# Performance work log

Hardware: AMD Instinct MI355X
Metric: run time of the kernel (lower is better)

The kernel has to match this reference:

```python
import jax, jax.numpy as jnp
import numpy as np

N_CELLS_PER_SIDE = 16
MAX_K = 32
N_HEADS = 8
CHUNK = 128

_NEIGHBOR_OFFSETS = jnp.array([[-1, -1], [-1, 0], [-1, 1], [0, -1], [0, 0], [0, 1], [1, -1], [1, 0], [1, 1]], dtype=jnp.int32)


def cell_lookup(query_pos, cell_map, pos_min, pos_range):
    B, S, _ = query_pos.shape
    mpc = cell_map.shape[1]
    normalized = (query_pos - pos_min) / pos_range
    cell_xy = jnp.clip((normalized * N_CELLS_PER_SIDE).astype(jnp.int32), 0, N_CELLS_PER_SIDE - 1)
    nb = jnp.clip(cell_xy[:, :, None, :] + _NEIGHBOR_OFFSETS[None, None, :, :], 0, N_CELLS_PER_SIDE - 1)
    nidx = nb[..., 0] * N_CELLS_PER_SIDE + nb[..., 1]
    cand = cell_map[nidx].reshape(B, S, 9 * mpc)
    valid = cand >= 0
    return jnp.where(valid, cand, 0), valid


def threshold_gate(scores, tau, max_k):
    raw = scores - tau
    gate = jnp.where(raw > 0, raw, 1e-8 * jnp.exp(raw))
    eg = jnp.exp(gate) - 1.0
    k = min(max_k, scores.shape[-1])
    tv, _ = jax.lax.top_k(eg, k)
    eg = jnp.where(eg >= tv[:, :, -1:], eg, 0.0)
    gs = eg.sum(axis=-1, keepdims=True) + 1e-8
    strength = jnp.tanh(eg.max(axis=-1, keepdims=True))
    return eg / gs * strength


def setup_inputs() -> dict:
    key = jax.random.key(0)
    ks = jax.random.split(key, 16)
    B, S, D, N, P = 2, 1024, 512, 4096, 2
    n_cells, mpc = N_CELLS_PER_SIDE ** 2, 32
    return {
        "x": jax.random.normal(ks[0], (B, S, D), jnp.float32),
        "qk_pos": jax.random.uniform(ks[1], (B, S, P), jnp.float32),
        "v_pos": jax.random.uniform(ks[2], (B, S, P), jnp.float32),
        "tau_Q": jax.random.uniform(ks[3], (B, S, 1), jnp.float32),
        "tau_K": jax.random.uniform(ks[4], (B, S, 1), jnp.float32),
        "tau_V": jax.random.uniform(ks[5], (B, S, 1), jnp.float32),
        "qk_neurons": jax.random.normal(ks[6], (N, D), jnp.float32) / np.float32(np.sqrt(D)),
        "v_neurons": jax.random.normal(ks[7], (N, D), jnp.float32) / np.float32(np.sqrt(D)),
        "npos_qk": jax.random.uniform(ks[8], (N, P), jnp.float32),
        "npos_v": jax.random.uniform(ks[9], (N, P), jnp.float32),
        "cell_map_qk": jax.random.randint(ks[10], (n_cells, mpc), 0, N, jnp.int32),
        "cell_map_v": jax.random.randint(ks[11], (n_cells, mpc), 0, N, jnp.int32),
        "pos_min": jnp.zeros((P,), jnp.float32),
        "pos_range": jnp.ones((P,), jnp.float32),
        "expand_O": jax.random.normal(ks[12], (D, D), jnp.float32) * 0.02,
    }


def reference(x, qk_pos, v_pos, tau_Q, tau_K, tau_V, qk_neurons, v_neurons, npos_qk, npos_v, cell_map_qk, cell_map_v, pos_min, pos_range, expand_O):
    B, S, D = x.shape
    # full-sequence spatial cell lookup (small int tensors)
    ci_qk, m_qk = cell_lookup(qk_pos, cell_map_qk, pos_min, pos_range)
    ci_v, m_v = cell_lookup(v_pos, cell_map_v, pos_min, pos_range)
    ci_qk = jax.lax.stop_gradient(ci_qk)
    ci_v = jax.lax.stop_gradient(ci_v)
    nc = S // CHUNK  # S chosen divisible by CHUNK (no padding path needed)

    def chunks(a):
        return a.reshape(B, nc, CHUNK, *a.shape[2:]).swapaxes(0, 1)

    inp = tuple(map(chunks, (x, qk_pos, v_pos, tau_Q, tau_K, tau_V, ci_qk, m_qk, ci_v, m_v)))

    def step(carry, c):
        x_c, qkp, vp, tq, tk, tv, i_qk, mk, i_v, mv = c
        cand_qk = qk_neurons[i_qk]  # [B,C,n_cand,D]
        cand_v = v_neurons[i_v]
        act_qk = jnp.einsum('bsd,bsnd->bsn', x_c, cand_qk)
        act_v = jnp.einsum('bsd,bsnd->bsn', x_c, cand_v)
        s_qk = jnp.where(mk, act_qk, -1e9)
        s_v = jnp.where(mv, act_v, -1e9)
        gQ = threshold_gate(s_qk, tq, MAX_K)
        gK = threshold_gate(s_qk, tk, MAX_K)
        gV = threshold_gate(s_v, tv, MAX_K)
        Q_c = jnp.einsum('bsn,bsnd->bsd', act_qk * gQ * mk, cand_qk)
        K_c = jnp.einsum('bsn,bsnd->bsd', act_qk * gK * mk, cand_qk)
        V_c = jnp.einsum('bsn,bsnd->bsd', act_v * gV * mv, cand_v)
        pd_qk = jnp.sum((qkp[:, :, None, :] - npos_qk[i_qk]) ** 2, axis=-1)
        pl_qk = (jax.lax.stop_gradient(gQ) * pd_qk * mk).sum() / (mk.sum() + 1e-8)
        pd_v = jnp.sum((vp[:, :, None, :] - npos_v[i_v]) ** 2, axis=-1)
        pl_v = (jax.lax.stop_gradient(gV) * pd_v * mv).sum() / (mv.sum() + 1e-8)
        return carry, (Q_c, K_c, V_c, pl_qk + pl_v)

    _, (Qs, Ks, Vs, pls) = jax.lax.scan(step, 0, inp)

    def merge(a):
        return a.swapaxes(0, 1).reshape(B, S, D)

    Q, K, V = merge(Qs), merge(Ks), merge(Vs)
    pos_loss = pls.mean()  # == sum / n_chunks

    dh = D // N_HEADS
    Qh = Q.reshape(B, S, N_HEADS, dh).transpose(0, 2, 1, 3)
    Kh = K.reshape(B, S, N_HEADS, dh).transpose(0, 2, 1, 3)
    Vh = V.reshape(B, S, N_HEADS, dh).transpose(0, 2, 1, 3)
    scores = jnp.einsum('bhsd,bhtd->bhst', Qh, Kh) / jnp.sqrt(jnp.float32(dh))
    causal = jnp.tril(jnp.ones((S, S), dtype=jnp.bool_))
    scores = jnp.where(causal, scores, jnp.finfo(scores.dtype).min)
    attn = jax.nn.softmax(scores, axis=-1)
    out = jnp.einsum('bhst,bhtd->bhsd', attn, Vh)
    out = out.transpose(0, 2, 1, 3).reshape(B, S, D)
    out = out @ expand_O
    return out, pos_loss
```

## Files before the change

### kernel.cpp

```cpp
#include <hip/hip_runtime.h>
#include <math.h>

#define B_ 2
#define S_ 1024
#define D_ 512
#define N_ 4096
#define H_ 8
#define DH_ 64
#define NCAND 288
#define TOPK 32
#define NTOK (B_*S_)
#define NG2 1152

#define NROWS 16384
#define NSLOT_BH 8704
#define NSLOTS (16*NSLOT_BH)

__device__ __forceinline__ float wave_sum(float v) {
    #pragma unroll
    for (int o = 32; o; o >>= 1) v += __shfl_xor(v, o);
    return v;
}
__device__ __forceinline__ float wave_max(float v) {
    #pragma unroll
    for (int o = 32; o; o >>= 1) v = fmaxf(v, __shfl_xor(v, o));
    return v;
}

__global__ __launch_bounds__(1024) void sort_tokens_kernel(
    const float* __restrict__ qk_pos, const float* __restrict__ v_pos,
    const float* __restrict__ pos_min, const float* __restrict__ pos_range,
    int* __restrict__ order_qk, int* __restrict__ order_v,
    int2* __restrict__ desc_qk, int2* __restrict__ desc_v)
{
    __shared__ int hist[256], tmp[256], offs[256], startc[256], gcnt[256];
    const int t = threadIdx.x;
    const int pass = blockIdx.x;
    const float pm0 = pos_min[0], pm1 = pos_min[1];
    const float pr0 = pos_range[0], pr1 = pos_range[1];
    const float* pos = pass ? v_pos : qk_pos;
    int* order = pass ? order_v : order_qk;
    int2* desc = pass ? desc_v : desc_qk;
    if (t < NG2) desc[t] = make_int2(0, 0);
    if (t + 1024 < NG2) desc[t + 1024] = make_int2(0, 0);
    if (t < 256) hist[t] = 0;
    __syncthreads();
    int cell[2];
    #pragma unroll
    for (int k = 0; k < 2; k++) {
        int tok = t + k * 1024;
        float p0 = pos[tok * 2], p1 = pos[tok * 2 + 1];
        int cx = min(max((int)((p0 - pm0) / pr0 * 16.f), 0), 15);
        int cy = min(max((int)((p1 - pm1) / pr1 * 16.f), 0), 15);
        cell[k] = cx * 16 + cy;
        atomicAdd(&hist[cell[k]], 1);
    }
    __syncthreads();
    if (t < 256) tmp[t] = hist[t];
    __syncthreads();
    for (int d = 1; d < 256; d <<= 1) {
        int v = 0;
        if (t < 256 && t >= d) v = tmp[t - d];
        __syncthreads();
        if (t < 256) tmp[t] += v;
        __syncthreads();
    }
    if (t < 256) {
        startc[t] = tmp[t] - hist[t];
        offs[t]   = startc[t];
        gcnt[t]   = (hist[t] + 1) >> 1;
    }
    __syncthreads();
    #pragma unroll
    for (int k = 0; k < 2; k++) {
        int tok = t + k * 1024;
        int p = atomicAdd(&offs[cell[k]], 1);
        order[p] = tok;
    }
    __syncthreads();
    if (t < 256) tmp[t] = gcnt[t];
    __syncthreads();
    for (int d = 1; d < 256; d <<= 1) {
        int v = 0;
        if (t < 256 && t >= d) v = tmp[t - d];
        __syncthreads();
        if (t < 256) tmp[t] += v;
        __syncthreads();
    }
    if (t < 256) {
        int g0 = tmp[t] - gcnt[t];
        for (int k = 0; k < gcnt[t]; k++)
            desc[g0 + k] = make_int2(startc[t] + 2 * k, min(2, hist[t] - 2 * k));
    }
}

__global__ __launch_bounds__(256) void qkv_fused(
    const int2* __restrict__ desc_qk, const int* __restrict__ order_qk,
    const int2* __restrict__ desc_v,  const int* __restrict__ order_v,
    const float* __restrict__ x,
    const float* __restrict__ qk_pos, const float* __restrict__ v_pos,
    const float* __restrict__ tauQ, const float* __restrict__ tauK,
    const float* __restrict__ tauV,
    const float* __restrict__ qk_neurons, const float* __restrict__ v_neurons,
    const float* __restrict__ npos_qk, const float* __restrict__ npos_v,
    const int* __restrict__ cm_qk, const int* __restrict__ cm_v,
    const float* __restrict__ pos_min, const float* __restrict__ pos_range,
    float* __restrict__ Q, float* __restrict__ K, float* __restrict__ V,
    float* __restrict__ posacc)
{
    const int bid = blockIdx.x;
    const int role = bid & 1;
    const int g = bid >> 1;
    const int gid = (g & 7) * 144 + (g >> 3);
    const int2 dsc = role ? desc_v[gid] : desc_qk[gid];
    const int gstart = dsc.x, count = dsc.y;
    if (count == 0) return;

    const int*   order   = role ? order_v   : order_qk;
    const float* pose    = role ? v_pos     : qk_pos;
    const float* neurons = role ? v_neurons : qk_neurons;
    const float* npos    = role ? npos_v    : npos_qk;
    const int*   cmap    = role ? cm_v      : cm_qk;

    __shared__ int   idx[NCAND];
    __shared__ float msk[NCAND];
    __shared__ float act[2][NCAND];
    __shared__ int   ci[2][NCAND];
    __shared__ float cw1[2][NCAND], cw2[2][NCAND];
    __shared__ int   toks[2], cnt2[2];
    __shared__ float red[2][2][4];
    __shared__ float redc;

    const int t = threadIdx.x, wid = t >> 6, lane = t & 63;
    const int sub = lane & 15, grp = lane >> 4;
    if (t < 2) { toks[t] = order[gstart + min(t, count - 1)]; cnt2[t] = 0; }
    __syncthreads();
    const int token0 = toks[0];

    const float pm0 = pos_min[0], pm1 = pos_min[1];
    const float pr0 = pos_range[0], pr1 = pos_range[1];
    {
        const float p0 = pose[token0 * 2], p1 = pose[token0 * 2 + 1];
        const int cx = min(max((int)((p0 - pm0) / pr0 * 16.f), 0), 15);
        const int cy = min(max((int)((p1 - pm1) / pr1 * 16.f), 0), 15);
        for (int c = t; c < NCAND; c += 256) {
            int o = c >> 5, ms = c & 31;
            int nx = min(max(cx + o / 3 - 1, 0), 15), ny = min(max(cy + o % 3 - 1, 0), 15);
            int cand = cmap[(nx * 16 + ny) * 32 + ms];
            idx[c] = cand >= 0 ? cand : 0;
            msk[c] = cand >= 0 ? 1.f : 0.f;
        }
    }
    __syncthreads();

    float4 xr0[8], xr1[8];
    {
        const float4* xp0 = (const float4*)(x + (size_t)toks[0] * D_);
        const float4* xp1 = (const float4*)(x + (size_t)toks[1] * D_);
        #pragma unroll
        for (int k = 0; k < 8; k++) {
            xr0[k] = xp0[k * 16 + sub];
            xr1[k] = xp1[k * 16 + sub];
        }
    }

    const int cb = wid * 72;
    for (int u = 0; u < 72; u += 4) {
        const int c = cb + u + grp;
        const float4* rp = (const float4*)(neurons + (size_t)idx[c] * D_);
        float a0 = 0.f, a1 = 0.f, b0 = 0.f, b1 = 0.f;
        #pragma unroll
        for (int k = 0; k < 8; k += 2) {
            float4 r0 = rp[k * 16 + sub];
            float4 r1 = rp[(k + 1) * 16 + sub];
            a0 += xr0[k].x*r0.x + xr0[k].y*r0.y + xr0[k].z*r0.z + xr0[k].w*r0.w;
            a1 += xr1[k].x*r0.x + xr1[k].y*r0.y + xr1[k].z*r0.z + xr1[k].w*r0.w;
            b0 += xr0[k+1].x*r1.x + xr0[k+1].y*r1.y + xr0[k+1].z*r1.z + xr0[k+1].w*r1.w;
            b1 += xr1[k+1].x*r1.x + xr1[k+1].y*r1.y + xr1[k+1].z*r1.z + xr1[k+1].w*r1.w;
        }
        float f0 = a0 + b0, f1 = a1 + b1;
        #pragma unroll
        for (int o = 1; o <= 8; o <<= 1) {
            f0 += __shfl_xor(f0, o);
            f1 += __shfl_xor(f1, o);
        }
        if (sub == 0) {
            const float mv = msk[c];
            act[0][c] = (mv != 0.f) ? f0 : -1e9f;
            act[1][c] = (mv != 0.f) ? f1 : -1e9f;
        }
    }
    __syncthreads();

    const int tk = wid >> 1, sw = wid & 1, tt = t & 127;
    const int token = toks[tk];

    if (sw == 0) {
        unsigned ej[5];
        #pragma unroll
        for (int k = 0; k < 5; k++) {
            int j = lane + 64 * k;
            float f = (j < NCAND) ? act[tk][j] : -1e30f;
            unsigned uu = __float_as_uint(f);
            ej[k] = (uu & 0x80000000u) ? ~uu : (uu | 0x80000000u);
        }
        unsigned T = 0u;
        for (int bit = 31; bit >= 0; bit--) {
            const unsigned cand = T | (1u << bit);
            int c = 0;
            #pragma unroll
            for (int k = 0; k < 5; k++)
                c += __popcll(__ballot(ej[k] >= cand));
            if (c >= TOPK) T = cand;
        }
        int base = 0;
        const unsigned long long below = (lane == 0) ? 0ull
                                       : (~0ull >> (64 - lane));
        #pragma unroll
        for (int k = 0; k < 5; k++) {
            const unsigned long long mk2 = __ballot(ej[k] >= T);
            if (ej[k] >= T) {
                int pos = base + __popcll(mk2 & below);
                ci[tk][pos] = lane + 64 * k;
            }
            base += __popcll(mk2);
        }
        if (lane == 0) cnt2[tk] = base;
    }
    if (wid == 0) {
        float cmv = 0.f;
        for (int c = lane; c < NCAND; c += 64) cmv += msk[c];
        cmv = wave_sum(cmv);
        if (lane == 0) redc = cmv;
    }
    __syncthreads();
    const float cm = redc;
    const int n = cnt2[tk];

    if (role == 0) {
        const float tq = tauQ[token], tkk = tauK[token];
        float sQ = 0.f, sK = 0.f, mQ = 0.f, mK = 0.f;
        for (int p = tt; p < n; p += 128) {
            float s = act[tk][ci[tk][p]];
            float rq = s - tq;
            float gq = (rq > 0.f) ? rq : 1e-8f * __expf(rq);
            float egq = __expf(gq) - 1.f;
            float rk = s - tkk;
            float gk = (rk > 0.f) ? rk : 1e-8f * __expf(rk);
            float egk = __expf(gk) - 1.f;
            cw1[tk][p] = egq; cw2[tk][p] = egk;
            sQ += egq; sK += egk;
            mQ = fmaxf(mQ, egq); mK = fmaxf(mK, egk);
        }
        sQ = wave_sum(sQ); mQ = wave_max(mQ);
        sK = wave_sum(sK); mK = wave_max(mK);
        if (lane == 0) {
            red[tk][sw][0] = sQ; red[tk][sw][1] = mQ;
            red[tk][sw][2] = sK; red[tk][sw][3] = mK;
        }
        __syncthreads();
        const float scQ = tanhf(fmaxf(red[tk][0][1], red[tk][1][1]))
                        / (red[tk][0][0] + red[tk][1][0] + 1e-8f);
        const float scK = tanhf(fmaxf(red[tk][0][3], red[tk][1][3]))
                        / (red[tk][0][2] + red[tk][1][2] + 1e-8f);
        __syncthreads();

        const float qp0 = pose[token * 2], qp1 = pose[token * 2 + 1];
        float plq = 0.f;
        for (int p = tt; p < n; p += 128) {
            int e = ci[tk][p];
            int id = idx[e];
            float m = msk[e], a = act[tk][e];
            float gq = cw1[tk][p] * scQ;
            cw1[tk][p] = a * gq * m;
            cw2[tk][p] = a * cw2[tk][p] * scK * m;
            ci[tk][p] = id;
            float d0 = qp0 - npos[id * 2], d1 = qp1 - npos[id * 2 + 1];
            plq += gq * (d0 * d0 + d1 * d1) * m;
        }
        plq = wave_sum(plq);
        if (lane == 0) red[tk][sw][0] = plq;
        __syncthreads();
        if (tt == 0 && tk < count) {
            int chunk = (token & 1023) >> 7;
            atomicAdd(&posacc[chunk], red[tk][0][0] + red[tk][1][0]);
            atomicAdd(&posacc[8 + chunk], cm);
        }

        if (tk < count) {
            float4 qa = {0,0,0,0}, ka = {0,0,0,0};
            int p = 0;
            for (; p + 1 < n; p += 2) {
                const float4 rA = *(const float4*)(neurons + (size_t)ci[tk][p] * D_ + tt * 4);
                const float4 rB = *(const float4*)(neurons + (size_t)ci[tk][p + 1] * D_ + tt * 4);
                const float wA = cw1[tk][p], bA = cw2[tk][p];
                const float wB = cw1[tk][p + 1], bB = cw2[tk][p + 1];
                qa.x += wA * rA.x + wB * rB.x; qa.y += wA * rA.y + wB * rB.y;
                qa.z += wA * rA.z + wB * rB.z; qa.w += wA * rA.w + wB * rB.w;
                ka.x += bA * rA.x + bB * rB.x; ka.y += bA * rA.y + bB * rB.y;
                ka.z += bA * rA.z + bB * rB.z; ka.w += bA * rA.w + bB * rB.w;
            }
            if (p < n) {
                const float4 rA = *(const float4*)(neurons + (size_t)ci[tk][p] * D_ + tt * 4);
                const float wA = cw1[tk][p], bA = cw2[tk][p];
                qa.x += wA * rA.x; qa.y += wA * rA.y; qa.z += wA * rA.z; qa.w += wA * rA.w;
                ka.x += bA * rA.x; ka.y += bA * rA.y; ka.z += bA * rA.z; ka.w += bA * rA.w;
            }
            *(float4*)(Q + (size_t)token * D_ + tt * 4) = qa;
            *(float4*)(K + (size_t)token * D_ + tt * 4) = ka;
        }
    } else {
        const float tv = tauV[token];
        float sV = 0.f, mV = 0.f;
        for (int p = tt; p < n; p += 128) {
            float s = act[tk][ci[tk][p]];
            float rv = s - tv;
            float gv = (rv > 0.f) ? rv : 1e-8f * __expf(rv);
            float egv = __expf(gv) - 1.f;
            cw1[tk][p] = egv;
            sV += egv; mV = fmaxf(mV, egv);
        }
        sV = wave_sum(sV); mV = wave_max(mV);
        if (lane == 0) { red[tk][sw][0] = sV; red[tk][sw][1] = mV; }
        __syncthreads();
        const float scV = tanhf(fmaxf(red[tk][0][1], red[tk][1][1]))
                        / (red[tk][0][0] + red[tk][1][0] + 1e-8f);
        __syncthreads();

        const float vp0 = pose[token * 2], vp1 = pose[token * 2 + 1];
        float plv = 0.f;
        for (int p = tt; p < n; p += 128) {
            int e = ci[tk][p];
            int id = idx[e];
            float m = msk[e], a = act[tk][e];
            float gv = cw1[tk][p] * scV;
            cw1[tk][p] = a * gv * m;
            ci[tk][p] = id;
            float d0 = vp0 - npos[id * 2], d1 = vp1 - npos[id * 2 + 1];
            plv += gv * (d0 * d0 + d1 * d1) * m;
        }
        plv = wave_sum(plv);
        if (lane == 0) red[tk][sw][0] = plv;
        __syncthreads();
        if (tt == 0 && tk < count) {
            int chunk = (token & 1023) >> 7;
            atomicAdd(&posacc[16 + chunk], red[tk][0][0] + red[tk][1][0]);
            atomicAdd(&posacc[24 + chunk], cm);
        }

        if (tk < count) {
            float4 va = {0,0,0,0};
            int p = 0;
            for (; p + 1 < n; p += 2) {
                const float4 rA = *(const float4*)(neurons + (size_t)ci[tk][p] * D_ + tt * 4);
                const float4 rB = *(const float4*)(neurons + (size_t)ci[tk][p + 1] * D_ + tt * 4);
                const float wA = cw1[tk][p], wB = cw1[tk][p + 1];
                va.x += wA * rA.x + wB * rB.x; va.y += wA * rA.y + wB * rB.y;
                va.z += wA * rA.z + wB * rB.z; va.w += wA * rA.w + wB * rB.w;
            }
            if (p < n) {
                const float4 rA = *(const float4*)(neurons + (size_t)ci[tk][p] * D_ + tt * 4);
                const float wA = cw1[tk][p];
                va.x += wA * rA.x; va.y += wA * rA.y; va.z += wA * rA.z; va.w += wA * rA.w;
            }
            *(float4*)(V + (size_t)token * D_ + tt * 4) = va;
        }
    }
}

typedef __attribute__((ext_vector_type(8))) short short8;
typedef __attribute__((ext_vector_type(4))) float f32x4;

__device__ __forceinline__ ushort f2b_rn(float f) {
    unsigned u = __float_as_uint(f);
    return (ushort)((u + 0x7FFFu + ((u >> 16) & 1u)) >> 16);
}
__device__ __forceinline__ float b2f(ushort h) {
    return __uint_as_float(((unsigned)h) << 16);
}
__device__ __forceinline__ int swzi(int row, int c8) {
    return row * 64 + ((c8 ^ (row & 7)) << 3);
}

__global__ __launch_bounds__(256, 2) void attn_partial_kernel(
    const float* __restrict__ Q, const float* __restrict__ K,
    const float* __restrict__ V,
    float* __restrict__ pm, float* __restrict__ pl, float* __restrict__ po)
{
    const int xx = blockIdx.x & 7;
    int kq = blockIdx.x >> 3;
    const int bh = xx + 8 * (kq >= 72);
    kq = (kq >= 72) ? kq - 72 : kq;
    int rblk = 0;
    while (kq >= 2 * (rblk + 1)) { kq -= 2 * (rblk + 1); rblk++; }
    const int sp = kq;
    const int b = bh >> 3, h = bh & 7;
    const int j0 = sp * 64;
    const int rbase = rblk * 128;

    __shared__ __align__(16) ushort sKhi[64 * 64], sKlo[64 * 64];
    __shared__ __align__(16) ushort sVthi[64 * 64], sVtlo[64 * 64];
    __shared__ __align__(16) float sPool[8192];

    const int t = threadIdx.x;
    const int w = t >> 6, lane = t & 63;
    const int g = lane >> 4, ln = lane & 15;

    {
        const int srow = t >> 2, scol = (t & 3) << 4;
        const float* Kg = K + ((size_t)(b * S_ + j0 + srow)) * D_ + h * DH_ + scol;
        const float* Vg = V + ((size_t)(b * S_ + j0 + srow)) * D_ + h * DH_ + scol;
        union { float4 f4[4]; float f[16]; } kf, vf;
        kf.f4[0] = *(const float4*)(Kg);
        kf.f4[1] = *(const float4*)(Kg + 4);
        kf.f4[2] = *(const float4*)(Kg + 8);
        kf.f4[3] = *(const float4*)(Kg + 12);
        vf.f4[0] = *(const float4*)(Vg);
        vf.f4[1] = *(const float4*)(Vg + 4);
        vf.f4[2] = *(const float4*)(Vg + 8);
        vf.f4[3] = *(const float4*)(Vg + 12);
        union { uint4 d[2]; ushort u[16]; } uh, ul;
        #pragma unroll
        for (int i = 0; i < 16; i++) {
            uh.u[i] = f2b_rn(kf.f[i]);
            ul.u[i] = f2b_rn(kf.f[i] - b2f(uh.u[i]));
        }
        const int c8 = (t & 3) << 1;
        *(uint4*)&sKhi[swzi(srow, c8)]     = uh.d[0];
        *(uint4*)&sKhi[swzi(srow, c8 + 1)] = uh.d[1];
        *(uint4*)&sKlo[swzi(srow, c8)]     = ul.d[0];
        *(uint4*)&sKlo[swzi(srow, c8 + 1)] = ul.d[1];
        #pragma unroll
        for (int i = 0; i < 16; i++) sPool[srow * 65 + scol + i] = vf.f[i];
    }
    __syncthreads();
    {
        const int drow = t >> 2, kcol = (t & 3) << 4;
        union { uint4 d[2]; ushort u[16]; } uh, ul;
        #pragma unroll
        for (int i = 0; i < 16; i++) {
            const float f = sPool[(kcol + i) * 65 + drow];
            uh.u[i] = f2b_rn(f);
            ul.u[i] = f2b_rn(f - b2f(uh.u[i]));
        }
        const int c8 = (t & 3) << 1;
        *(uint4*)&sVthi[swzi(drow, c8)]     = uh.d[0];
        *(uint4*)&sVthi[swzi(drow, c8 + 1)] = uh.d[1];
        *(uint4*)&sVtlo[swzi(drow, c8)]     = ul.d[0];
        *(uint4*)&sVtlo[swzi(drow, c8 + 1)] = ul.d[1];
    }
    __syncthreads();

    const int wrow = rbase + w * 32;
    if (wrow + 31 < j0) return;

    ushort* sPw = (ushort*)sPool + w * 4096;

    short8 qhi[2][2], qlo[2][2];
    #pragma unroll
    for (int qt = 0; qt < 2; qt++) {
        const int qrow = wrow + qt * 16 + ln;
        const float* Qg = Q + ((size_t)(b * S_ + qrow)) * D_ + h * DH_ + g * 8;
        #pragma unroll
        for (int ds = 0; ds < 2; ds++) {
// ... 74 lines not shown
            const int c8 = kt * 2 + (g >> 1);
            const int idx = qrow * 64 + ((c8 ^ (qrow & 7)) << 3) + ((g & 1) << 2);
            *(uint2*)&sPw[idx] = h4.d;
            *(uint2*)&sPw[2048 + idx] = l4.d;
        }
        if (g == 0 && qg >= j0) {
            const int gr = qg >> 6;
            const size_t slot = (size_t)bh * NSLOT_BH + 32 * gr * (gr + 1)
                              + (size_t)(qg & 63) * (gr + 1) + sp;
            pm[slot] = mq; pl[slot] = lq;
        }
    }

    f32x4 ot[4][2];
    #pragma unroll
    for (int dt = 0; dt < 4; dt++)
        #pragma unroll
        for (int qt = 0; qt < 2; qt++)
            ot[dt][qt] = fzero;
    #pragma unroll
    for (int ks = 0; ks < 2; ks++) {
        short8 pfh[2], pfl[2];
        #pragma unroll
        for (int qt = 0; qt < 2; qt++) {
            const int qrow = qt * 16 + ln;
            const int idx = qrow * 64 + (((ks * 4 + g) ^ (qrow & 7)) << 3);
            pfh[qt] = *(const short8*)&sPw[idx];
            pfl[qt] = *(const short8*)&sPw[2048 + idx];
        }
        #pragma unroll
        for (int dt = 0; dt < 4; dt++) {
            const int drow = dt * 16 + ln;
            const short8 vh = *(const short8*)&sVthi[swzi(drow, ks * 4 + g)];
            const short8 vl = *(const short8*)&sVtlo[swzi(drow, ks * 4 + g)];
            #pragma unroll
            for (int qt = 0; qt < 2; qt++) {
                ot[dt][qt] = __builtin_amdgcn_mfma_f32_16x16x32_bf16(vh, pfh[qt], ot[dt][qt], 0, 0, 0);
                ot[dt][qt] = __builtin_amdgcn_mfma_f32_16x16x32_bf16(vh, pfl[qt], ot[dt][qt], 0, 0, 0);
                ot[dt][qt] = __builtin_amdgcn_mfma_f32_16x16x32_bf16(vl, pfh[qt], ot[dt][qt], 0, 0, 0);
            }
        }
    }

    #pragma unroll
    for (int qt = 0; qt < 2; qt++) {
        const int qg = wrow + qt * 16 + ln;
        if (qg < j0) continue;
        const int gr = qg >> 6;
        const size_t slot = (size_t)bh * NSLOT_BH + 32 * gr * (gr + 1)
                          + (size_t)(qg & 63) * (gr + 1) + sp;
        float* od = po + slot * 64 + g * 4;
        #pragma unroll
        for (int dt = 0; dt < 4; dt++)
            *(f32x4*)(od + dt * 16) = ot[dt][qt];
    }
}

__global__ __launch_bounds__(256) void attn_combine_kernel(
    const float* __restrict__ pm, const float* __restrict__ pl,
    const float* __restrict__ po, float* __restrict__ AO)
{
    const int gth = blockIdx.x * 256 + threadIdx.x;
    const int r = gth >> 6, d = gth & 63;
    const int i = r & 1023, bh = r >> 10;
    const int b = bh >> 3, h = bh & 7;
    const int g = i >> 6;
    const int ns = g + 1;
    const size_t slot0 = (size_t)bh * NSLOT_BH + 32 * g * (g + 1)
                       + (size_t)(i & 63) * (g + 1);
    float mstar = -INFINITY, lstar = 0.f, ostar = 0.f;
    for (int s = 0; s < ns; s++) {
        const float mi = pm[slot0 + s];
        const float nm = fmaxf(mstar, mi);
        const float a = __expf(mstar - nm);
        const float w = __expf(mi - nm);
        lstar = lstar * a + pl[slot0 + s] * w;
        ostar = ostar * a + po[(slot0 + s) * 64 + d] * w;
        mstar = nm;
    }
    AO[((size_t)(b * S_ + i)) * D_ + h * DH_ + d] = ostar / lstar;
}

__global__ __launch_bounds__(256) void proj_kernel(
    const float* __restrict__ A, const float* __restrict__ W,
    float* __restrict__ out)
{
    __shared__ float rows[4][D_];
    const int blk = blockIdx.x;
    const int t = threadIdx.x;
    {
        const float4* af = (const float4*)(A + (size_t)blk * 4 * D_);
        float4* rf = (float4*)&rows[0][0];
        rf[t] = af[t]; rf[t + 256] = af[t + 256];
    }
    __syncthreads();
    float acc0[4] = {0,0,0,0}, acc1[4] = {0,0,0,0};
    for (int d = 0; d < D_; d += 4) {
        float r0[4], r1[4], r2[4], r3[4];
        *(float4*)r0 = *(const float4*)&rows[0][d];
        *(float4*)r1 = *(const float4*)&rows[1][d];
        *(float4*)r2 = *(const float4*)&rows[2][d];
        *(float4*)r3 = *(const float4*)&rows[3][d];
        #pragma unroll
        for (int j = 0; j < 4; j++) {
            float w0 = W[(size_t)(d + j) * D_ + t];
            float w1 = W[(size_t)(d + j) * D_ + t + 256];
            acc0[0] += r0[j] * w0; acc1[0] += r0[j] * w1;
            acc0[1] += r1[j] * w0; acc1[1] += r1[j] * w1;
            acc0[2] += r2[j] * w0; acc1[2] += r2[j] * w1;
            acc0[3] += r3[j] * w0; acc1[3] += r3[j] * w1;
        }
    }
    #pragma unroll
    for (int k = 0; k < 4; k++) {
        const size_t base = (size_t)(blk * 4 + k) * D_;
        out[base + t] = acc0[k];
        out[base + t + 256] = acc1[k];
    }
}

__global__ void zero_acc_kernel(float* acc) {
    if (threadIdx.x < 32) acc[threadIdx.x] = 0.f;
}
__global__ void ploss_kernel(const float* __restrict__ acc, float* __restrict__ out) {
    float ssum = 0.f;
    for (int c = 0; c < 8; c++) {
        ssum += acc[c]      / (acc[8 + c]  + 1e-8f);
        ssum += acc[16 + c] / (acc[24 + c] + 1e-8f);
    }
    out[0] = ssum * 0.125f;
}

extern "C" void kernel_launch(void* const* d_in, const int* in_sizes, int n_in,
                              void* d_out, int out_size, void* d_ws, size_t ws_size,
                              hipStream_t stream) {
    const float* x          = (const float*)d_in[0];
    const float* qk_pos     = (const float*)d_in[1];
    const float* v_pos      = (const float*)d_in[2];
    const float* tauQ       = (const float*)d_in[3];
    const float* tauK       = (const float*)d_in[4];
    const float* tauV       = (const float*)d_in[5];
    const float* qk_neurons = (const float*)d_in[6];
    const float* v_neurons  = (const float*)d_in[7];
    const float* npos_qk    = (const float*)d_in[8];
    const float* npos_v     = (const float*)d_in[9];
    const int*   cm_qk      = (const int*)d_in[10];
    const int*   cm_v       = (const int*)d_in[11];
    const float* pos_min    = (const float*)d_in[12];
    const float* pos_range  = (const float*)d_in[13];
    const float* expand_O   = (const float*)d_in[14];

    float* ws = (float*)d_ws;
    const size_t TDf = (size_t)NTOK * D_;
    float* Q   = ws;
    float* K   = ws + TDf;
    float* V   = ws + 2 * TDf;
    float* AO  = ws + 3 * TDf;
    float* acc = ws + 4 * TDf;
    int*   order_qk = (int*)(ws + 4 * TDf + 64);
    int*   order_v  = order_qk + NTOK;
    int2*  desc_qk  = (int2*)(order_v + NTOK);
    int2*  desc_v   = desc_qk + NG2;
    const size_t head = 4 * TDf + 64 + 2 * NTOK + 4 * NG2;

    float* pm = ws + head;
    float* pl = pm + (size_t)NSLOTS;
    float* po = pl + (size_t)NSLOTS;

    float* out = (float*)d_out;

    zero_acc_kernel<<<1, 64, 0, stream>>>(acc);
    sort_tokens_kernel<<<2, 1024, 0, stream>>>(qk_pos, v_pos, pos_min, pos_range,
                                               order_qk, order_v, desc_qk, desc_v);
    qkv_fused<<<2 * NG2, 256, 0, stream>>>(desc_qk, order_qk, desc_v, order_v,
                                           x, qk_pos, v_pos, tauQ, tauK, tauV,
                                           qk_neurons, v_neurons, npos_qk, npos_v,
                                           cm_qk, cm_v, pos_min, pos_range,
                                           Q, K, V, acc);
    attn_partial_kernel<<<1152, 256, 0, stream>>>(Q, K, V, pm, pl, po);
    attn_combine_kernel<<<(NROWS * 64) / 256, 256, 0, stream>>>(pm, pl, po, AO);
    proj_kernel<<<NTOK / 4, 256, 0, stream>>>(AO, expand_O, out);
    ploss_kernel<<<1, 1, 0, stream>>>(acc, out + TDf);
}
```

Baseline: 266.5 us.

## Group eight same-cell tokens per block to reuse candidate neuron rows

Tokens are now bucketed in groups of up to 8 per spatial cell instead of 2, so one block scores 8 tokens against the shared 288 candidate neuron rows. Each wave now owns a token pair and runs its own top-k and gather, which drops the cross-wave shared-memory reductions and most block barriers. Candidate row loads are double-buffered in registers. The aim is to cut redundant global reads of neuron rows and per-block overhead, at the cost of larger shared-memory arrays, more register pressure and fewer blocks in flight.

```diff
diff --git a/kernel.cpp b/kernel.cpp
--- a/kernel.cpp
+++ b/kernel.cpp
@@ -10,7 +10,7 @@
 #define NCAND 288
 #define TOPK 32
 #define NTOK (B_*S_)
-#define NG2 1152
+#define NG8 512
 
 #define NROWS 16384
 #define NSLOT_BH 8704
@@ -25,6 +25,9 @@
     #pragma unroll
     for (int o = 32; o; o >>= 1) v = fmaxf(v, __shfl_xor(v, o));
     return v;
+}
+__device__ __forceinline__ void fma4(float4& a, float s, const float4 b) {
+    a.x += s * b.x; a.y += s * b.y; a.z += s * b.z; a.w += s * b.w;
 }
 
 __global__ __launch_bounds__(1024) void sort_tokens_kernel(
@@ -41,8 +44,7 @@
     const float* pos = pass ? v_pos : qk_pos;
     int* order = pass ? order_v : order_qk;
     int2* desc = pass ? desc_v : desc_qk;
-    if (t < NG2) desc[t] = make_int2(0, 0);
-    if (t + 1024 < NG2) desc[t + 1024] = make_int2(0, 0);
+    if (t < NG8) desc[t] = make_int2(0, 0);
     if (t < 256) hist[t] = 0;
     __syncthreads();
     int cell[2];
@@ -68,7 +70,7 @@
     if (t < 256) {
         startc[t] = tmp[t] - hist[t];
         offs[t]   = startc[t];
-        gcnt[t]   = (hist[t] + 1) >> 1;
+        gcnt[t]   = (hist[t] + 7) >> 3;
     }
     __syncthreads();
     #pragma unroll
@@ -90,8 +92,41 @@
     if (t < 256) {
         int g0 = tmp[t] - gcnt[t];
         for (int k = 0; k < gcnt[t]; k++)
-            desc[g0 + k] = make_int2(startc[t] + 2 * k, min(2, hist[t] - 2 * k));
-    }
+            desc[g0 + k] = make_int2(startc[t] + 8 * k, min(8, hist[t] - 8 * k));
+    }
+}
+
+__device__ __forceinline__ int rank_topk(const float* __restrict__ actRow,
+                                         int* __restrict__ ciRow, int lane) {
+    unsigned ej[5];
+    #pragma unroll
+    for (int k = 0; k < 5; k++) {
+        int j = lane + 64 * k;
+        float f = (j < NCAND) ? actRow[j] : -1e30f;
+        unsigned uu = __float_as_uint(f);
+        ej[k] = (uu & 0x80000000u) ? ~uu : (uu | 0x80000000u);
+    }
+    unsigned T = 0u;
+    for (int bit = 31; bit >= 0; bit--) {
+        const unsigned cand = T | (1u << bit);
+        int c = 0;
+        #pragma unroll
+        for (int k = 0; k < 5; k++)
+            c += __popcll(__ballot(ej[k] >= cand));
+        if (c >= TOPK) T = cand;
+    }
+    int base = 0;
+    const unsigned long long below = (lane == 0) ? 0ull : (~0ull >> (64 - lane));
+    #pragma unroll
+    for (int k = 0; k < 5; k++) {
+        const unsigned long long mk2 = __ballot(ej[k] >= T);
+        if (ej[k] >= T) {
+            int pos = base + __popcll(mk2 & below);
+            ciRow[pos] = lane + 64 * k;
+        }
+        base += __popcll(mk2);
+    }
+    return base;
 }
 
 __global__ __launch_bounds__(256) void qkv_fused(
@@ -110,8 +145,7 @@
 {
     const int bid = blockIdx.x;
     const int role = bid & 1;
-    const int g = bid >> 1;
-    const int gid = (g & 7) * 144 + (g >> 3);
+    const int gid = bid >> 1;
     const int2 dsc = role ? desc_v[gid] : desc_qk[gid];
     const int gstart = dsc.x, count = dsc.y;
     if (count == 0) return;
@@ -124,16 +158,14 @@
 
     __shared__ int   idx[NCAND];
     __shared__ float msk[NCAND];
-    __shared__ float act[2][NCAND];
-    __shared__ int   ci[2][NCAND];
-    __shared__ float cw1[2][NCAND], cw2[2][NCAND];
-    __shared__ int   toks[2], cnt2[2];
-    __shared__ float red[2][2][4];
-    __shared__ float redc;
+    __shared__ float act[8][NCAND];
+    __shared__ int   ci[8][NCAND];
+    __shared__ float cw1[8][NCAND], cw2[8][NCAND];
+    __shared__ int   toks[8];
 
     const int t = threadIdx.x, wid = t >> 6, lane = t & 63;
     const int sub = lane & 15, grp = lane >> 4;
-    if (t < 2) { toks[t] = order[gstart + min(t, count - 1)]; cnt2[t] = 0; }
+    if (t < 8) toks[t] = order[gstart + min(t, count - 1)];
     __syncthreads();
     const int token0 = toks[0];
 
@@ -153,10 +185,11 @@
     }
     __syncthreads();
 
+    const int tokA = 2 * grp, tokB = 2 * grp + 1;
     float4 xr0[8], xr1[8];
     {
-        const float4* xp0 = (const float4*)(x + (size_t)toks[0] * D_);
-        const float4* xp1 = (const float4*)(x + (size_t)toks[1] * D_);
+        const float4* xp0 = (const float4*)(x + (size_t)toks[tokA] * D_);
+        const float4* xp1 = (const float4*)(x + (size_t)toks[tokB] * D_);
         #pragma unroll
         for (int k = 0; k < 8; k++) {
             xr0[k] = xp0[k * 16 + sub];
@@ -164,206 +197,188 @@
         }
     }
 
-    const int cb = wid * 72;
-    for (int u = 0; u < 72; u += 4) {
-        const int c = cb + u + grp;
-        const float4* rp = (const float4*)(neurons + (size_t)idx[c] * D_);
-        float a0 = 0.f, a1 = 0.f, b0 = 0.f, b1 = 0.f;
-        #pragma unroll
-        for (int k = 0; k < 8; k += 2) {
-            float4 r0 = rp[k * 16 + sub];
-            float4 r1 = rp[(k + 1) * 16 + sub];
-            a0 += xr0[k].x*r0.x + xr0[k].y*r0.y + xr0[k].z*r0.z + xr0[k].w*r0.w;
-            a1 += xr1[k].x*r0.x + xr1[k].y*r0.y + xr1[k].z*r0.z + xr1[k].w*r0.w;
-            b0 += xr0[k+1].x*r1.x + xr0[k+1].y*r1.y + xr0[k+1].z*r1.z + xr0[k+1].w*r1.w;
-            b1 += xr1[k+1].x*r1.x + xr1[k+1].y*r1.y + xr1[k+1].z*r1.z + xr1[k+1].w*r1.w;
-        }
-        float f0 = a0 + b0, f1 = a1 + b1;
-        #pragma unroll
-        for (int o = 1; o <= 8; o <<= 1) {
-            f0 += __shfl_xor(f0, o);
-            f1 += __shfl_xor(f1, o);
-        }
-        if (sub == 0) {
-            const float mv = msk[c];
-            act[0][c] = (mv != 0.f) ? f0 : -1e9f;
-            act[1][c] = (mv != 0.f) ? f1 : -1e9f;
-        }
-    }
-    __syncthreads();
-
-    const int tk = wid >> 1, sw = wid & 1, tt = t & 127;
-    const int token = toks[tk];
-
-    if (sw == 0) {
-        unsigned ej[5];
-        #pragma unroll
-        for (int k = 0; k < 5; k++) {
-            int j = lane + 64 * k;
-            float f = (j < NCAND) ? act[tk][j] : -1e30f;
-            unsigned uu = __float_as_uint(f);
-            ej[k] = (uu & 0x80000000u) ? ~uu : (uu | 0x80000000u);
-        }
-        unsigned T = 0u;
-        for (int bit = 31; bit >= 0; bit--) {
-            const unsigned cand = T | (1u << bit);
-            int c = 0;
-            #pragma unroll
-            for (int k = 0; k < 5; k++)
-                c += __popcll(__ballot(ej[k] >= cand));
-            if (c >= TOPK) T = cand;
-        }
-        int base = 0;
-        const unsigned long long below = (lane == 0) ? 0ull
-                                       : (~0ull >> (64 - lane));
-        #pragma unroll
-        for (int k = 0; k < 5; k++) {
-            const unsigned long long mk2 = __ballot(ej[k] >= T);
-            if (ej[k] >= T) {
-                int pos = base + __popcll(mk2 & below);
-                ci[tk][pos] = lane + 64 * k;
-            }
-            base += __popcll(mk2);
-        }
-        if (lane == 0) cnt2[tk] = base;
-    }
-    if (wid == 0) {
-        float cmv = 0.f;
-        for (int c = lane; c < NCAND; c += 64) cmv += msk[c];
-        cmv = wave_sum(cmv);
-        if (lane == 0) redc = cmv;
-    }
-    __syncthreads();
-    const float cm = redc;
-    const int n = cnt2[tk];
+    #define LOADROW(buf, c) do { \
+        const float4* rp_ = (const float4*)(neurons + (size_t)idx[c] * D_); \
+        _Pragma("unroll") \
+        for (int k_ = 0; k_ < 8; k_++) buf[k_] = rp_[k_ * 16 + sub]; \
+    } while (0)
+    #define DOTSTORE(buf, c) do { \
+        float f0_ = 0.f, f1_ = 0.f; \
+        _Pragma("unroll") \
+        for (int k_ = 0; k_ < 8; k_++) { \
+            f0_ += xr0[k_].x*buf[k_].x + xr0[k_].y*buf[k_].y + xr0[k_].z*buf[k_].z + xr0[k_].w*buf[k_].w; \
+            f1_ += xr1[k_].x*buf[k_].x + xr1[k_].y*buf[k_].y + xr1[k_].z*buf[k_].z + xr1[k_].w*buf[k_].w; \
+        } \
+        _Pragma("unroll") \
+        for (int o_ = 1; o_ <= 8; o_ <<= 1) { \
+            f0_ += __shfl_xor(f0_, o_); \
+            f1_ += __shfl_xor(f1_, o_); \
+        } \
+        if (sub == 0) { \
+            const float mv_ = msk[c]; \
+            act[tokA][c] = (mv_ != 0.f) ? f0_ : -1e9f; \
+            act[tokB][c] = (mv_ != 0.f) ? f1_ : -1e9f; \
+        } \
+    } while (0)
+
+    {
+        const int cb = wid * 72;
+        float4 bufA[8], bufB[8];
+        LOADROW(bufA, cb);
+        for (int u = 0; u < 72; u += 2) {
+            LOADROW(bufB, cb + u + 1);
+            DOTSTORE(bufA, cb + u);
+            if (u + 2 < 72) LOADROW(bufA, cb + u + 2);
+            DOTSTORE(bufB, cb + u + 1);
+        }
+    }
+    __syncthreads();
+
+    float cmv = 0.f;
+    for (int c = lane; c < NCAND; c += 64) cmv += msk[c];
+    const float cm = wave_sum(cmv);
+
+    int n0 = 0, n1 = 0;
+    if (2 * wid < count)     n0 = rank_topk(act[2 * wid],     ci[2 * wid],     lane);
+    if (2 * wid + 1 < count) n1 = rank_topk(act[2 * wid + 1], ci[2 * wid + 1], lane);
 
     if (role == 0) {
-        const float tq = tauQ[token], tkk = tauK[token];
-        float sQ = 0.f, sK = 0.f, mQ = 0.f, mK = 0.f;
-        for (int p = tt; p < n; p += 128) {
-            float s = act[tk][ci[tk][p]];
-            float rq = s - tq;
-            float gq = (rq > 0.f) ? rq : 1e-8f * __expf(rq);
-            float egq = __expf(gq) - 1.f;
-            float rk = s - tkk;
-            float gk = (rk > 0.f) ? rk : 1e-8f * __expf(rk);
-            float egk = __expf(gk) - 1.f;
-            cw1[tk][p] = egq; cw2[tk][p] = egk;
-            sQ += egq; sK += egk;
-            mQ = fmaxf(mQ, egq); mK = fmaxf(mK, egk);
-        }
-        sQ = wave_sum(sQ); mQ = wave_max(mQ);
-        sK = wave_sum(sK); mK = wave_max(mK);
-        if (lane == 0) {
-            red[tk][sw][0] = sQ; red[tk][sw][1] = mQ;
-            red[tk][sw][2] = sK; red[tk][sw][3] = mK;
-        }
-        __syncthreads();
-        const float scQ = tanhf(fmaxf(red[tk][0][1], red[tk][1][1]))
-                        / (red[tk][0][0] + red[tk][1][0] + 1e-8f);
-        const float scK = tanhf(fmaxf(red[tk][0][3], red[tk][1][3]))
-                        / (red[tk][0][2] + red[tk][1][2] + 1e-8f);
-        __syncthreads();
-
-        const float qp0 = pose[token * 2], qp1 = pose[token * 2 + 1];
-        float plq = 0.f;
-        for (int p = tt; p < n; p += 128) {
-            int e = ci[tk][p];
-            int id = idx[e];
-            float m = msk[e], a = act[tk][e];
-            float gq = cw1[tk][p] * scQ;
-            cw1[tk][p] = a * gq * m;
-            cw2[tk][p] = a * cw2[tk][p] * scK * m;
-            ci[tk][p] = id;
-            float d0 = qp0 - npos[id * 2], d1 = qp1 - npos[id * 2 + 1];
-            plq += gq * (d0 * d0 + d1 * d1) * m;
-        }
-        plq = wave_sum(plq);
-        if (lane == 0) red[tk][sw][0] = plq;
-        __syncthreads();
-        if (tt == 0 && tk < count) {
-            int chunk = (token & 1023) >> 7;
-            atomicAdd(&posacc[chunk], red[tk][0][0] + red[tk][1][0]);
-            atomicAdd(&posacc[8 + chunk], cm);
-        }
-
-        if (tk < count) {
-            float4 qa = {0,0,0,0}, ka = {0,0,0,0};
+        #pragma unroll
+        for (int i = 0; i < 2; i++) {
+            const int tk = 2 * wid + i;
+            if (tk >= count) continue;
+            const int n = i ? n1 : n0;
+            const int token = toks[tk];
+            const float tq = tauQ[token], tkk = tauK[token];
+            float sQ = 0.f, sK = 0.f, mQ = 0.f, mK = 0.f;
+            for (int p = lane; p < n; p += 64) {
+                float s = act[tk][ci[tk][p]];
+                float rq = s - tq;
+                float gq = (rq > 0.f) ? rq : 1e-8f * __expf(rq);
+                float egq = __expf(gq) - 1.f;
+                float rk = s - tkk;
+                float gk = (rk > 0.f) ? rk : 1e-8f * __expf(rk);
+                float egk = __expf(gk) - 1.f;
+                cw1[tk][p] = egq; cw2[tk][p] = egk;
+                sQ += egq; sK += egk;
+                mQ = fmaxf(mQ, egq); mK = fmaxf(mK, egk);
+            }
+            sQ = wave_sum(sQ); mQ = wave_max(mQ);
+            sK = wave_sum(sK); mK = wave_max(mK);
+            const float scQ = tanhf(mQ) / (sQ + 1e-8f);
+            const float scK = tanhf(mK) / (sK + 1e-8f);
+
+            const float qp0 = pose[token * 2], qp1 = pose[token * 2 + 1];
+            float plq = 0.f;
+            for (int p = lane; p < n; p += 64) {
+                int e = ci[tk][p];
+                int id = idx[e];
+                float m = msk[e], a = act[tk][e];
+                float gq = cw1[tk][p] * scQ;
+                cw1[tk][p] = a * gq * m;
+                cw2[tk][p] = a * cw2[tk][p] * scK * m;
+                ci[tk][p] = id;
+                float d0 = qp0 - npos[id * 2], d1 = qp1 - npos[id * 2 + 1];
+                plq += gq * (d0 * d0 + d1 * d1) * m;
+            }
+            plq = wave_sum(plq);
+            if (lane == 0) {
+                int chunk = (token & 1023) >> 7;
+                atomicAdd(&posacc[chunk], plq);
+                atomicAdd(&posacc[8 + chunk], cm);
+            }
+
+            float4 qa0 = {0,0,0,0}, qa1 = {0,0,0,0};
+            float4 ka0 = {0,0,0,0}, ka1 = {0,0,0,0};
             int p = 0;
             for (; p + 1 < n; p += 2) {
-                const float4 rA = *(const float4*)(neurons + (size_t)ci[tk][p] * D_ + tt * 4);
-                const float4 rB = *(const float4*)(neurons + (size_t)ci[tk][p + 1] * D_ + tt * 4);
+                const float* rA = neurons + (size_t)ci[tk][p] * D_ + lane * 8;
+                const float* rB = neurons + (size_t)ci[tk][p + 1] * D_ + lane * 8;
+                const float4 A0 = *(const float4*)rA;
+                const float4 A1 = *(const float4*)(rA + 4);
+                const float4 B0 = *(const float4*)rB;
+                const float4 B1 = *(const float4*)(rB + 4);
                 const float wA = cw1[tk][p], bA = cw2[tk][p];
                 const float wB = cw1[tk][p + 1], bB = cw2[tk][p + 1];
-                qa.x += wA * rA.x + wB * rB.x; qa.y += wA * rA.y + wB * rB.y;
-                qa.z += wA * rA.z + wB * rB.z; qa.w += wA * rA.w + wB * rB.w;
-                ka.x += bA * rA.x + bB * rB.x; ka.y += bA * rA.y + bB * rB.y;
-                ka.z += bA * rA.z + bB * rB.z; ka.w += bA * rA.w + bB * rB.w;
+                fma4(qa0, wA, A0); fma4(qa0, wB, B0);
+                fma4(qa1, wA, A1); fma4(qa1, wB, B1);
+                fma4(ka0, bA, A0); fma4(ka0, bB, B0);
+                fma4(ka1, bA, A1); fma4(ka1, bB, B1);
             }
             if (p < n) {
-                const float4 rA = *(const float4*)(neurons + (size_t)ci[tk][p] * D_ + tt * 4);
+                const float* rA = neurons + (size_t)ci[tk][p] * D_ + lane * 8;
+                const float4 A0 = *(const float4*)rA;
+                const float4 A1 = *(const float4*)(rA + 4);
                 const float wA = cw1[tk][p], bA = cw2[tk][p];
-                qa.x += wA * rA.x; qa.y += wA * rA.y; qa.z += wA * rA.z; qa.w += wA * rA.w;
-                ka.x += bA * rA.x; ka.y += bA * rA.y; ka.z += bA * rA.z; ka.w += bA * rA.w;
-            }
-            *(float4*)(Q + (size_t)token * D_ + tt * 4) = qa;
-            *(float4*)(K + (size_t)token * D_ + tt * 4) = ka;
+                fma4(qa0, wA, A0); fma4(qa1, wA, A1);
+                fma4(ka0, bA, A0); fma4(ka1, bA, A1);
+            }
+            *(float4*)(Q + (size_t)token * D_ + lane * 8)     = qa0;
+            *(float4*)(Q + (size_t)token * D_ + lane * 8 + 4) = qa1;
+            *(float4*)(K + (size_t)token * D_ + lane * 8)     = ka0;
+            *(float4*)(K + (size_t)token * D_ + lane * 8 + 4) = ka1;
         }
     } else {
-        const float tv = tauV[token];
-        float sV = 0.f, mV = 0.f;
-        for (int p = tt; p < n; p += 128) {
-            float s = act[tk][ci[tk][p]];
-            float rv = s - tv;
-            float gv = (rv > 0.f) ? rv : 1e-8f * __expf(rv);
-            float egv = __expf(gv) - 1.f;
-            cw1[tk][p] = egv;
-            sV += egv; mV = fmaxf(mV, egv);
-        }
-        sV = wave_sum(sV); mV = wave_max(mV);
-        if (lane == 0) { red[tk][sw][0] = sV; red[tk][sw][1] = mV; }
-        __syncthreads();
-        const float scV = tanhf(fmaxf(red[tk][0][1], red[tk][1][1]))
-                        / (red[tk][0][0] + red[tk][1][0] + 1e-8f);
-        __syncthreads();
-
-        const float vp0 = pose[token * 2], vp1 = pose[token * 2 + 1];
-        float plv = 0.f;
-        for (int p = tt; p < n; p += 128) {
-            int e = ci[tk][p];
-            int id = idx[e];
-            float m = msk[e], a = act[tk][e];
-            float gv = cw1[tk][p] * scV;
-            cw1[tk][p] = a * gv * m;
-            ci[tk][p] = id;
-            float d0 = vp0 - npos[id * 2], d1 = vp1 - npos[id * 2 + 1];
-            plv += gv * (d0 * d0 + d1 * d1) * m;
-        }
-        plv = wave_sum(plv);
-        if (lane == 0) red[tk][sw][0] = plv;
-        __syncthreads();
-        if (tt == 0 && tk < count) {
-            int chunk = (token & 1023) >> 7;
-            atomicAdd(&posacc[16 + chunk], red[tk][0][0] + red[tk][1][0]);
-            atomicAdd(&posacc[24 + chunk], cm);
-        }
-
-        if (tk < count) {
-            float4 va = {0,0,0,0};
+        #pragma unroll
+        for (int i = 0; i < 2; i++) {
+            const int tk = 2 * wid + i;
+            if (tk >= count) continue;
+            const int n = i ? n1 : n0;
+            const int token = toks[tk];
+            const float tv = tauV[token];
+            float sV = 0.f, mV = 0.f;
+            for (int p = lane; p < n; p += 64) {
+                float s = act[tk][ci[tk][p]];
+                float rv = s - tv;
+                float gv = (rv > 0.f) ? rv : 1e-8f * __expf(rv);
+                float egv = __expf(gv) - 1.f;
+                cw1[tk][p] = egv;
+                sV += egv; mV = fmaxf(mV, egv);
+            }
+            sV = wave_sum(sV); mV = wave_max(mV);
+            const float scV = tanhf(mV) / (sV + 1e-8f);
+
+            const float vp0 = pose[token * 2], vp1 = pose[token * 2 + 1];
+            float plv = 0.f;
+            for (int p = lane; p < n; p += 64) {
+                int e = ci[tk][p];
+                int id = idx[e];
+                float m = msk[e], a = act[tk][e];
+                float gv = cw1[tk][p] * scV;
+                cw1[tk][p] = a * gv * m;
+                ci[tk][p] = id;
+                float d0 = vp0 - npos[id * 2], d1 = vp1 - npos[id * 2 + 1];
+                plv += gv * (d0 * d0 + d1 * d1) * m;
+            }
+            plv = wave_sum(plv);
+            if (lane == 0) {
+                int chunk = (token & 1023) >> 7;
+                atomicAdd(&posacc[16 + chunk], plv);
+                atomicAdd(&posacc[24 + chunk], cm);
+            }
+
+            float4 va0 = {0,0,0,0}, va1 = {0,0,0,0};
             int p = 0;
             for (; p + 1 < n; p += 2) {
-                const float4 rA = *(const float4*)(neurons + (size_t)ci[tk][p] * D_ + tt * 4);
-                const float4 rB = *(const float4*)(neurons + (size_t)ci[tk][p + 1] * D_ + tt * 4);
+                const float* rA = neurons + (size_t)ci[tk][p] * D_ + lane * 8;
+                const float* rB = neurons + (size_t)ci[tk][p + 1] * D_ + lane * 8;
+                const float4 A0 = *(const float4*)rA;
+                const float4 A1 = *(const float4*)(rA + 4);
+                const float4 B0 = *(const float4*)rB;
+                const float4 B1 = *(const float4*)(rB + 4);
                 const float wA = cw1[tk][p], wB = cw1[tk][p + 1];
-                va.x += wA * rA.x + wB * rB.x; va.y += wA * rA.y + wB * rB.y;
-                va.z += wA * rA.z + wB * rB.z; va.w += wA * rA.w + wB * rB.w;
+                fma4(va0, wA, A0); fma4(va0, wB, B0);
+                fma4(va1, wA, A1); fma4(va1, wB, B1);
             }
             if (p < n) {
-                const float4 rA = *(const float4*)(neurons + (size_t)ci[tk][p] * D_ + tt * 4);
+                const float* rA = neurons + (size_t)ci[tk][p] * D_ + lane * 8;
+                const float4 A0 = *(const float4*)rA;
+                const float4 A1 = *(const float4*)(rA + 4);
                 const float wA = cw1[tk][p];
-                va.x += wA * rA.x; va.y += wA * rA.y; va.z += wA * rA.z; va.w += wA * rA.w;
-            }
-            *(float4*)(V + (size_t)token * D_ + tt * 4) = va;
+                fma4(va0, wA, A0); fma4(va1, wA, A1);
+            }
+            *(float4*)(V + (size_t)token * D_ + lane * 8)     = va0;
+            *(float4*)(V + (size_t)token * D_ + lane * 8 + 4) = va1;
         }
     }
 }
@@ -698,8 +713,8 @@
     int*   order_qk = (int*)(ws + 4 * TDf + 64);
     int*   order_v  = order_qk + NTOK;
     int2*  desc_qk  = (int2*)(order_v + NTOK);
-    int2*  desc_v   = desc_qk + NG2;
-    const size_t head = 4 * TDf + 64 + 2 * NTOK + 4 * NG2;
+    int2*  desc_v   = desc_qk + NG8;
+    const size_t head = 4 * TDf + 64 + 2 * NTOK + 4 * NG8;
 
     float* pm = ws + head;
     float* pl = pm + (size_t)NSLOTS;
@@ -710,7 +725,7 @@
     zero_acc_kernel<<<1, 64, 0, stream>>>(acc);
     sort_tokens_kernel<<<2, 1024, 0, stream>>>(qk_pos, v_pos, pos_min, pos_range,
                                                order_qk, order_v, desc_qk, desc_v);
-    qkv_fused<<<2 * NG2, 256, 0, stream>>>(desc_qk, order_qk, desc_v, order_v,
+    qkv_fused<<<2 * NG8, 256, 0, stream>>>(desc_qk, order_qk, desc_v, order_v,
                                            x, qk_pos, v_pos, tauQ, tauK, tauV,
                                            qk_neurons, v_neurons, npos_qk, npos_v,
                                            cm_qk, cm_v, pos_min, pos_range,
```

Result: slower. 286.5 us (+7.5%).

## Move output projection to split-bf16 MFMA and fold accumulator zeroing into sort

Applied to the files above, without the earlier changes.

The scalar FP32 output projection is replaced by an MFMA kernel. A and W are each split into high and low bf16 parts, and three 16x16x32 bf16 MFMAs approximate FP32 accuracy. A new wprep kernel transposes expand_O and splits it into bf16 hi/lo arrays in the workspace on every call. The separate zero-accumulator launch is folded into sort_tokens_kernel to save one launch. The cost is an extra prep kernel each call and a small precision loss from the 3-term bf16 split.

```diff
diff --git a/kernel.cpp b/kernel.cpp
--- a/kernel.cpp
+++ b/kernel.cpp
@@ -16,6 +16,9 @@
 #define NSLOT_BH 8704
 #define NSLOTS (16*NSLOT_BH)
 
+typedef __attribute__((ext_vector_type(8))) short short8;
+typedef __attribute__((ext_vector_type(4))) float f32x4;
+
 __device__ __forceinline__ float wave_sum(float v) {
     #pragma unroll
     for (int o = 32; o; o >>= 1) v += __shfl_xor(v, o);
@@ -25,17 +28,29 @@
     #pragma unroll
     for (int o = 32; o; o >>= 1) v = fmaxf(v, __shfl_xor(v, o));
     return v;
+}
+__device__ __forceinline__ ushort f2b_rn(float f) {
+    unsigned u = __float_as_uint(f);
+    return (ushort)((u + 0x7FFFu + ((u >> 16) & 1u)) >> 16);
+}
+__device__ __forceinline__ float b2f(ushort h) {
+    return __uint_as_float(((unsigned)h) << 16);
+}
+__device__ __forceinline__ int swzi(int row, int c8) {
+    return row * 64 + ((c8 ^ (row & 7)) << 3);
 }
 
 __global__ __launch_bounds__(1024) void sort_tokens_kernel(
     const float* __restrict__ qk_pos, const float* __restrict__ v_pos,
     const float* __restrict__ pos_min, const float* __restrict__ pos_range,
     int* __restrict__ order_qk, int* __restrict__ order_v,
-    int2* __restrict__ desc_qk, int2* __restrict__ desc_v)
+    int2* __restrict__ desc_qk, int2* __restrict__ desc_v,
+    float* __restrict__ posacc)
 {
     __shared__ int hist[256], tmp[256], offs[256], startc[256], gcnt[256];
     const int t = threadIdx.x;
     const int pass = blockIdx.x;
+    if (pass == 0 && t < 32) posacc[t] = 0.f;
     const float pm0 = pos_min[0], pm1 = pos_min[1];
     const float pr0 = pos_range[0], pr1 = pos_range[1];
     const float* pos = pass ? v_pos : qk_pos;
@@ -368,18 +383,32 @@
     }
 }
 
-typedef __attribute__((ext_vector_type(8))) short short8;
-typedef __attribute__((ext_vector_type(4))) float f32x4;
-
-__device__ __forceinline__ ushort f2b_rn(float f) {
-    unsigned u = __float_as_uint(f);
-    return (ushort)((u + 0x7FFFu + ((u >> 16) & 1u)) >> 16);
-}
-__device__ __forceinline__ float b2f(ushort h) {
-    return __uint_as_float(((unsigned)h) << 16);
-}
-__device__ __forceinline__ int swzi(int row, int c8) {
-    return row * 64 + ((c8 ^ (row & 7)) << 3);
+__global__ __launch_bounds__(256) void wprep_kernel(
+    const float* __restrict__ W, ushort* __restrict__ Wth, ushort* __restrict__ Wtl)
+{
+    __shared__ float tile[64][65];
+    const int bx = blockIdx.x & 7, by = blockIdx.x >> 3;
+    const int t = threadIdx.x;
+    const int r = t >> 4, c4 = (t & 15) * 4;
+    #pragma unroll
+    for (int rr = 0; rr < 64; rr += 16) {
+        const float4 v = *(const float4*)(W + (size_t)(by * 64 + rr + r) * 512 + bx * 64 + c4);
+        *(float4*)&tile[rr + r][c4] = v;
+    }
+    __syncthreads();
+    #pragma unroll
+    for (int cc = 0; cc < 64; cc += 16) {
+        const int c = cc + r;
+        ushort h[4], l[4];
+        #pragma unroll
+        for (int i = 0; i < 4; i++) {
+            float f = tile[c4 + i][c];
+            h[i] = f2b_rn(f);
+            l[i] = f2b_rn(f - b2f(h[i]));
+        }
+        *(uint2*)&Wth[(size_t)(bx * 64 + c) * 512 + by * 64 + c4] = *(uint2*)h;
+        *(uint2*)&Wtl[(size_t)(bx * 64 + c) * 512 + by * 64 + c4] = *(uint2*)l;
+    }
 }
 
 __global__ __launch_bounds__(256, 2) void attn_partial_kernel(
@@ -620,46 +649,52 @@
 }
 
 __global__ __launch_bounds__(256) void proj_kernel(
-    const float* __restrict__ A, const float* __restrict__ W,
+    const float* __restrict__ A,
+    const ushort* __restrict__ Wth, const ushort* __restrict__ Wtl,
     float* __restrict__ out)
 {
-    __shared__ float rows[4][D_];
-    const int blk = blockIdx.x;
-    const int t = threadIdx.x;
-    {
-        const float4* af = (const float4*)(A + (size_t)blk * 4 * D_);
-        float4* rf = (float4*)&rows[0][0];
-        rf[t] = af[t]; rf[t + 256] = af[t + 256];
-    }
-    __syncthreads();
-    float acc0[4] = {0,0,0,0}, acc1[4] = {0,0,0,0};
-    for (int d = 0; d < D_; d += 4) {
-        float r0[4], r1[4], r2[4], r3[4];
-        *(float4*)r0 = *(const float4*)&rows[0][d];
-        *(float4*)r1 = *(const float4*)&rows[1][d];
-        *(float4*)r2 = *(const float4*)&rows[2][d];
-        *(float4*)r3 = *(const float4*)&rows[3][d];
-        #pragma unroll
-        for (int j = 0; j < 4; j++) {
-            float w0 = W[(size_t)(d + j) * D_ + t];
-            float w1 = W[(size_t)(d + j) * D_ + t + 256];
-            acc0[0] += r0[j] * w0; acc1[0] += r0[j] * w1;
-            acc0[1] += r1[j] * w0; acc1[1] += r1[j] * w1;
-            acc0[2] += r2[j] * w0; acc1[2] += r2[j] * w1;
-            acc0[3] += r3[j] * w0; acc1[3] += r3[j] * w1;
-        }
-    }
-    #pragma unroll
-    for (int k = 0; k < 4; k++) {
-        const size_t base = (size_t)(blk * 4 + k) * D_;
-        out[base + t] = acc0[k];
-        out[base + t + 256] = acc1[k];
-    }
-}
-
-__global__ void zero_acc_kernel(float* acc) {
-    if (threadIdx.x < 32) acc[threadIdx.x] = 0.f;
-}
+    const int tb = (blockIdx.x >> 4) * 64;
+    const int cb = (blockIdx.x & 15) * 32;
+    const int t = threadIdx.x, w = t >> 6, lane = t & 63;
+    const int ln = lane & 15, ko = (lane >> 4) * 8;
+    const int tok = tb + w * 16 + ln;
+
+    const f32x4 fz = {0.f, 0.f, 0.f, 0.f};
+    f32x4 acc[2];
+    acc[0] = fz; acc[1] = fz;
+
+    const float* Ap = A + (size_t)tok * 512 + ko;
+    #pragma unroll 4
+    for (int ks = 0; ks < 512; ks += 32) {
+        union { float4 f4[2]; float f[8]; } af;
+        af.f4[0] = *(const float4*)(Ap + ks);
+        af.f4[1] = *(const float4*)(Ap + ks + 4);
+        union { short8 v; ushort u[8]; } ah, al;
+        #pragma unroll
+        for (int i = 0; i < 8; i++) {
+            ah.u[i] = f2b_rn(af.f[i]);
+            al.u[i] = f2b_rn(af.f[i] - b2f(ah.u[i]));
+        }
+        #pragma unroll
+        for (int ct = 0; ct < 2; ct++) {
+            const size_t wb = (size_t)(cb + ct * 16 + ln) * 512 + ks + ko;
+            const short8 bh = *(const short8*)(Wth + wb);
+            const short8 bl = *(const short8*)(Wtl + wb);
+            acc[ct] = __builtin_amdgcn_mfma_f32_16x16x32_bf16(ah.v, bh, acc[ct], 0, 0, 0);
+            acc[ct] = __builtin_amdgcn_mfma_f32_16x16x32_bf16(al.v, bh, acc[ct], 0, 0, 0);
+            acc[ct] = __builtin_amdgcn_mfma_f32_16x16x32_bf16(ah.v, bl, acc[ct], 0, 0, 0);
+        }
+    }
+    #pragma unroll
+    for (int ct = 0; ct < 2; ct++) {
+        #pragma unroll
+        for (int r = 0; r < 4; r++) {
+            const int row = tb + w * 16 + (lane >> 4) * 4 + r;
+            out[(size_t)row * 512 + cb + ct * 16 + ln] = acc[ct][r];
+        }
+    }
+}
+
 __global__ void ploss_kernel(const float* __restrict__ acc, float* __restrict__ out) {
     float ssum = 0.f;
     for (int c = 0; c < 8; c++) {
@@ -704,12 +739,15 @@
     float* pm = ws + head;
     float* pl = pm + (size_t)NSLOTS;
     float* po = pl + (size_t)NSLOTS;
+    ushort* Wth = (ushort*)(po + (size_t)NSLOTS * 64);
+    ushort* Wtl = Wth + 512 * 512;
 
     float* out = (float*)d_out;
 
-    zero_acc_kernel<<<1, 64, 0, stream>>>(acc);
     sort_tokens_kernel<<<2, 1024, 0, stream>>>(qk_pos, v_pos, pos_min, pos_range,
-                                               order_qk, order_v, desc_qk, desc_v);
+                                               order_qk, order_v, desc_qk, desc_v,
+                                               acc);
+    wprep_kernel<<<64, 256, 0, stream>>>(expand_O, Wth, Wtl);
     qkv_fused<<<2 * NG2, 256, 0, stream>>>(desc_qk, order_qk, desc_v, order_v,
                                            x, qk_pos, v_pos, tauQ, tauK, tauV,
                                            qk_neurons, v_neurons, npos_qk, npos_v,
@@ -717,6 +755,6 @@
                                            Q, K, V, acc);
     attn_partial_kernel<<<1152, 256, 0, stream>>>(Q, K, V, pm, pl, po);
     attn_combine_kernel<<<(NROWS * 64) / 256, 256, 0, stream>>>(pm, pl, po, AO);
-    proj_kernel<<<NTOK / 4, 256, 0, stream>>>(AO, expand_O, out);
+    proj_kernel<<<512, 256, 0, stream>>>(AO, Wth, Wtl, out);
     ploss_kernel<<<1, 1, 0, stream>>>(acc, out + TDf);
 }
```

Measured after the change: 256.0 us. -3.9%, faster.
